# Performance work log

Hardware: AMD Instinct MI355X
Metric: run time of the kernel (lower is better)

The kernel has to match this reference:

```python
import jax, jax.numpy as jnp
import numpy as np

T = 2048          # tokens (single causal prefill sequence)
H = 4096          # hidden_size
NH = 32           # num query heads
NKV = 8           # num kv heads (GQA)
HD = H // NH      # head_dim = 128
ROPE_THETA = 500000.0
Q_SIZE = NH * HD
KV_SIZE = NKV * HD


def setup_inputs() -> dict:
    key = jax.random.key(0)
    k1, k2, k3 = jax.random.split(key, 3)
    return {
        "positions": jnp.arange(T, dtype=jnp.int32),
        "hidden_states": jax.random.normal(k1, (T, H), dtype=jnp.float32) * 0.02,
        "w_qkv": jax.random.normal(k2, (H, Q_SIZE + 2 * KV_SIZE), dtype=jnp.float32) * (1.0 / np.sqrt(H)),
        "w_o": jax.random.normal(k3, (Q_SIZE, H), dtype=jnp.float32) * (1.0 / np.sqrt(Q_SIZE)),
    }


def _apply_rope(x, positions):
    # x: [T, heads, HD]; neox-style (non-interleaved) RoPE as in get_rope
    half = HD // 2
    inv_freq = 1.0 / (ROPE_THETA ** (jnp.arange(0, half, dtype=jnp.float32) / half * 1.0))
    # note: standard llama uses arange(0, HD, 2)/HD == arange(half)/half
    freqs = positions.astype(jnp.float32)[:, None] * inv_freq[None, :]   # [T, half]
    cos = jnp.cos(freqs)[:, None, :]  # [T, 1, half]
    sin = jnp.sin(freqs)[:, None, :]
    x1, x2 = x[..., :half], x[..., half:]
    return jnp.concatenate([x1 * cos - x2 * sin, x2 * cos + x1 * sin], axis=-1).astype(x.dtype)


def reference(positions, hidden_states, w_qkv, w_o):
    # qkv_proj (no bias)
    qkv = hidden_states @ w_qkv                               # [T, 6144]
    q, k, v = jnp.split(qkv, [Q_SIZE, Q_SIZE + KV_SIZE], axis=-1)
    q = q.reshape(T, NH, HD)
    k = k.reshape(T, NKV, HD)
    v = v.reshape(T, NKV, HD)

    # fused RoPE on q and k (k would be written rotated into the KV cache)
    q = _apply_rope(q, positions)
    k = _apply_rope(k, positions)

    # GQA: expand kv heads to query heads
    group = NH // NKV
    k_rep = jnp.repeat(k, group, axis=1)                      # [T, NH, HD]
    v_rep = jnp.repeat(v, group, axis=1)

    scale = HD ** -0.5
    scores = jnp.einsum('qhd,shd->hqs', q, k_rep) * scale     # [NH, T, T]
    causal = jnp.tril(jnp.ones((T, T), dtype=bool))
    scores = jnp.where(causal[None], scores, jnp.finfo(scores.dtype).min)
    probs = jax.nn.softmax(scores, axis=-1)
    attn = jnp.einsum('hqs,shd->qhd', probs, v_rep)           # [T, NH, HD]

    out = attn.reshape(T, Q_SIZE) @ w_o                       # o_proj
    return out
```

## Files before the change

### kernel.cpp

```cpp
#include <hip/hip_runtime.h>
#include <cstdint>
#include <cstddef>

#define T_SEQ 2048
#define H_DIM 4096
#define NH 32
#define NKV 8
#define HD 128
#define QKV_N 6144
#define Q_SIZE 4096
#define KV_SIZE 1024

typedef __attribute__((ext_vector_type(8))) short bf16x8;
typedef __attribute__((ext_vector_type(4))) short short4v;
typedef __attribute__((ext_vector_type(4))) float f32x4;

__device__ __forceinline__ short f2bf(float f) {
  union { float f; uint32_t u; } v; v.f = f;
  uint32_t r = v.u + 0x7fffu + ((v.u >> 16) & 1u);
  return (short)(r >> 16);
}

__device__ __forceinline__ void gload_lds16(const void* g, void* l) {
  __builtin_amdgcn_global_load_lds((const __attribute__((address_space(1))) void*)g,
                                   (__attribute__((address_space(3))) void*)l,
                                   16, 0, 0);
}

__global__ __launch_bounds__(256) void cvt_bf16_kernel(const float* __restrict__ in,
                                                       short* __restrict__ out, int n4) {
  int i = blockIdx.x * 256 + threadIdx.x;
  if (i < n4) {
    float4 v = ((const float4*)in)[i];
    short4v s;
    s.x = f2bf(v.x); s.y = f2bf(v.y); s.z = f2bf(v.z); s.w = f2bf(v.w);
    ((short4v*)out)[i] = s;
  }
}

__global__ __launch_bounds__(256) void transpose_cvt_kernel(const float* __restrict__ in,
                                                            short* __restrict__ out,
                                                            int rows, int cols) {
  __shared__ float tile[32][33];
  int bx = blockIdx.x * 32;
  int by = blockIdx.y * 32;
  int x = threadIdx.x, y = threadIdx.y;
#pragma unroll
  for (int i = 0; i < 32; i += 8)
    tile[y + i][x] = in[(size_t)(by + y + i) * cols + bx + x];
  __syncthreads();
#pragma unroll
  for (int i = 0; i < 32; i += 8)
    out[(size_t)(bx + y + i) * rows + by + x] = f2bf(tile[x][y + i]);
}

__global__ __launch_bounds__(256) void gemm_bt_kernel(const short* __restrict__ A,
                                                      const short* __restrict__ Bt,
                                                      float* __restrict__ C,
                                                      int M, int N, int K) {
  __shared__ short As[128 * 32];
  __shared__ short Bs[128 * 32];
  int tid = threadIdx.x;
  int w = tid >> 6, lane = tid & 63;
  int quad = lane >> 4, l16 = lane & 15;
  int wm = (w >> 1) * 64, wn = (w & 1) * 64;
  int bm = blockIdx.y * 128, bn = blockIdx.x * 128;
  f32x4 acc[4][4] = {};
  for (int kk = 0; kk < K; kk += 32) {
    __syncthreads();
#pragma unroll
    for (int p = 0; p < 2; ++p) {
      int e = (p * 256 + tid) * 8;
      int row = e >> 5, kc = e & 31;
      gload_lds16(A + (size_t)(bm + row) * K + kk + kc, As + e);
      gload_lds16(Bt + (size_t)(bn + row) * K + kk + kc, Bs + e);
    }
    __syncthreads();
    bf16x8 af[4], bfr[4];
#pragma unroll
    for (int mi = 0; mi < 4; ++mi)
      af[mi] = *(const bf16x8*)(As + (wm + mi * 16 + l16) * 32 + quad * 8);
#pragma unroll
    for (int ni = 0; ni < 4; ++ni)
      bfr[ni] = *(const bf16x8*)(Bs + (wn + ni * 16 + l16) * 32 + quad * 8);
#pragma unroll
    for (int mi = 0; mi < 4; ++mi)
#pragma unroll
      for (int ni = 0; ni < 4; ++ni)
        acc[mi][ni] = __builtin_amdgcn_mfma_f32_16x16x32_bf16(af[mi], bfr[ni], acc[mi][ni], 0, 0, 0);
  }
#pragma unroll
  for (int mi = 0; mi < 4; ++mi)
#pragma unroll
    for (int ni = 0; ni < 4; ++ni) {
      int r0 = bm + wm + mi * 16 + quad * 4;
      int c0 = bn + wn + ni * 16 + l16;
#pragma unroll
      for (int r = 0; r < 4; ++r)
        C[(size_t)(r0 + r) * N + c0] = acc[mi][ni][r];
    }
}

__global__ __launch_bounds__(256) void rope_kernel(const float* __restrict__ qkv,
                                                   const int* __restrict__ positions,
                                                   short* __restrict__ qb,
                                                   short* __restrict__ kb) {
  int t = blockIdx.x;
  int hh = blockIdx.y * 4 + (threadIdx.x >> 6);
  int j = threadIdx.x & 63;
  float pos = (float)positions[t];
  float f = pos * exp2f(-(float)j * 0.29580575889569017f);
  float c = cosf(f), sn = sinf(f);
  size_t rowbase = (size_t)t * QKV_N;
  int coloff = (hh < NH) ? hh * HD : Q_SIZE + (hh - NH) * HD;
  float x1 = qkv[rowbase + coloff + j];
  float x2 = qkv[rowbase + coloff + j + 64];
  float o1 = x1 * c - x2 * sn;
  float o2 = x2 * c + x1 * sn;
  const float scale2 = 0.08838834764831845f * 1.4426950408889634f;
  short* dst;
  if (hh < NH) {
    o1 *= scale2; o2 *= scale2;
    dst = qb + ((size_t)hh * T_SEQ + t) * HD;
  } else {
    dst = kb + ((size_t)(hh - NH) * T_SEQ + t) * HD;
  }
  dst[j] = f2bf(o1);
  dst[j + 64] = f2bf(o2);
}

__global__ __launch_bounds__(256) void transpose_v_kernel(const float* __restrict__ qkv,
                                                          short* __restrict__ vt) {
  __shared__ float tile[32][33];
  int bx = blockIdx.x * 32;
  int by = blockIdx.y * 32;
  int x = threadIdx.x, y = threadIdx.y;
#pragma unroll
  for (int i = 0; i < 32; i += 8)
    tile[y + i][x] = qkv[(size_t)(by + y + i) * QKV_N + (Q_SIZE + KV_SIZE) + bx + x];
  __syncthreads();
#pragma unroll
  for (int i = 0; i < 32; i += 8)
    vt[(size_t)(bx + y + i) * T_SEQ + by + x] = f2bf(tile[x][y + i]);
}

#define PS_STR 72
__global__ __launch_bounds__(256, 2) void flash_kernel(const short* __restrict__ qb,
                                                       const short* __restrict__ kb,
                                                       const short* __restrict__ vt,
                                                       short* __restrict__ attn) {
  __shared__ short Ks[64 * 128];
  __shared__ short Vs[128 * 64];
  __shared__ short Ps[8][16 * PS_STR];
  int c = (int)gridDim.x - 1 - (int)blockIdx.x;
  int h = blockIdx.y;
  int kvh = h >> 2;
  int tid = threadIdx.x;
  int w = tid >> 6, lane = tid & 63;
  int quad = lane >> 4, l16 = lane & 15;
  int qrow0w = c * 128 + w * 32;

  const short* kbh = kb + (size_t)kvh * T_SEQ * HD;
  const short* vth = vt + (size_t)kvh * HD * T_SEQ;

  bf16x8 qf[2][4];
#pragma unroll
  for (int g = 0; g < 2; ++g) {
    const short* qbase = qb + ((size_t)h * T_SEQ + qrow0w + g * 16 + l16) * HD + quad * 8;
#pragma unroll
    for (int dk = 0; dk < 4; ++dk) qf[g][dk] = *(const bf16x8*)(qbase + dk * 32);
  }
  f32x4 o[2][8] = {};
  float lp[2] = {0.0f, 0.0f};

  int ktmax_blk = 2 * c + 2;
  int ktmax_w = 2 * c + 1 + (w >> 1);

  for (int kt = 0; kt < ktmax_blk; ++kt) {
    int kpos0 = kt * 64;
    __syncthreads();
#pragma unroll
    for (int p4 = 0; p4 < 4; ++p4) {
      int e = p4 * 256 + tid;
      int kr = e >> 4, kp = e & 15;
      gload_lds16(kbh + (size_t)(kpos0 + kr) * HD + ((kp ^ (kr & 7)) * 8), Ks + e * 8);
      int vd = e >> 3, vp = e & 7;
      gload_lds16(vth + (size_t)vd * T_SEQ + kpos0 + ((vp ^ (vd & 7)) * 8), Vs + e * 8);
    }
    __syncthreads();
    if (kt >= ktmax_w) continue;

    f32x4 s[2][4] = {};
#pragma unroll
    for (int mi = 0; mi < 4; ++mi) {
      int kr = mi * 16 + l16;
      const short* kfb = Ks + kr * 128;
      int sw = kr & 7;
#pragma unroll
      for (int dk = 0; dk < 4; ++dk) {
        bf16x8 kf = *(const bf16x8*)(kfb + (((dk * 4 + quad) ^ sw) * 8));
        s[0][mi] = __builtin_amdgcn_mfma_f32_16x16x32_bf16(kf, qf[0][dk], s[0][mi], 0, 0, 0);
        s[1][mi] = __builtin_amdgcn_mfma_f32_16x16x32_bf16(kf, qf[1][dk], s[1][mi], 0, 0, 0);
      }
    }
#pragma unroll
    for (int g = 0; g < 2; ++g) {
      int qr = qrow0w + g * 16 + l16;
      bool need_mask = (kpos0 + 63 > qrow0w + g * 16);
#pragma unroll
      for (int mi = 0; mi < 4; ++mi) {
        float p0, p1, p2, p3;
        if (need_mask) {
          int kp = kpos0 + mi * 16 + quad * 4;
          p0 = exp2f((kp + 0 > qr) ? -1e30f : s[g][mi][0]);
          p1 = exp2f((kp + 1 > qr) ? -1e30f : s[g][mi][1]);
          p2 = exp2f((kp + 2 > qr) ? -1e30f : s[g][mi][2]);
          p3 = exp2f((kp + 3 > qr) ? -1e30f : s[g][mi][3]);
        } else {
          p0 = exp2f(s[g][mi][0]); p1 = exp2f(s[g][mi][1]);
          p2 = exp2f(s[g][mi][2]); p3 = exp2f(s[g][mi][3]);
        }
        lp[g] += p0 + p1 + p2 + p3;
        short4v pk;
        pk.x = f2bf(p0); pk.y = f2bf(p1); pk.z = f2bf(p2); pk.w = f2bf(p3);
        *(short4v*)(&Ps[w * 2 + g][l16 * PS_STR + mi * 16 + quad * 4]) = pk;
      }
    }
#pragma unroll
    for (int kf2 = 0; kf2 < 2; ++kf2) {
      bf16x8 pf0 = *(const bf16x8*)(&Ps[w * 2 + 0][l16 * PS_STR + kf2 * 32 + quad * 8]);
      bf16x8 pf1 = *(const bf16x8*)(&Ps[w * 2 + 1][l16 * PS_STR + kf2 * 32 + quad * 8]);
#pragma unroll
      for (int ni = 0; ni < 8; ++ni) {
        int vd = ni * 16 + l16;
        bf16x8 vf = *(const bf16x8*)(Vs + vd * 64 + (((kf2 * 4 + quad) ^ (vd & 7)) * 8));
        o[0][ni] = __builtin_amdgcn_mfma_f32_16x16x32_bf16(vf, pf0, o[0][ni], 0, 0, 0);
        o[1][ni] = __builtin_amdgcn_mfma_f32_16x16x32_bf16(vf, pf1, o[1][ni], 0, 0, 0);
      }
    }
  }
#pragma unroll
  for (int g = 0; g < 2; ++g) {
    float lt = lp[g];
    lt += __shfl_xor(lt, 16, 64);
    lt += __shfl_xor(lt, 32, 64);
    float rl = 1.0f / lt;
    short* dst = attn + (size_t)(qrow0w + g * 16 + l16) * Q_SIZE + h * HD + quad * 4;
#pragma unroll
    for (int ni = 0; ni < 8; ++ni) {
      short4v ov;
      ov.x = f2bf(o[g][ni][0] * rl); ov.y = f2bf(o[g][ni][1] * rl);
      ov.z = f2bf(o[g][ni][2] * rl); ov.w = f2bf(o[g][ni][3] * rl);
      *(short4v*)(dst + ni * 16) = ov;
    }
  }
}

extern "C" void kernel_launch(void* const* d_in, const int* in_sizes, int n_in,
                              void* d_out, int out_size, void* d_ws, size_t ws_size,
                              hipStream_t stream) {
  const int* positions = (const int*)d_in[0];
  const float* hidden  = (const float*)d_in[1];
  const float* w_qkv   = (const float*)d_in[2];
  const float* w_o     = (const float*)d_in[3];
  float* out = (float*)d_out;

  char* p = (char*)d_ws;
  short* hA    = (short*)p;               short* attn = hA;
  p += (size_t)T_SEQ * H_DIM * 2;
  short* wqkvT = (short*)p;
  p += (size_t)QKV_N * H_DIM * 2;
  float* qkv   = (float*)p;               short* woT = (short*)p;
  short* qb = wqkvT;
  short* kb = qb + (size_t)NH * T_SEQ * HD;
  short* vt = kb + (size_t)NKV * T_SEQ * HD;

  cvt_bf16_kernel<<<dim3(T_SEQ * H_DIM / 4 / 256), 256, 0, stream>>>(hidden, hA, T_SEQ * H_DIM / 4);
  transpose_cvt_kernel<<<dim3(QKV_N / 32, H_DIM / 32), dim3(32, 8), 0, stream>>>(w_qkv, wqkvT, H_DIM, QKV_N);
  gemm_bt_kernel<<<dim3(QKV_N / 128, T_SEQ / 128), 256, 0, stream>>>(hA, wqkvT, qkv, T_SEQ, QKV_N, H_DIM);
  rope_kernel<<<dim3(T_SEQ, (NH + NKV) / 4), 256, 0, stream>>>(qkv, positions, qb, kb);
  transpose_v_kernel<<<dim3(KV_SIZE / 32, T_SEQ / 32), dim3(32, 8), 0, stream>>>(qkv, vt);
  transpose_cvt_kernel<<<dim3(H_DIM / 32, H_DIM / 32), dim3(32, 8), 0, stream>>>(w_o, woT, H_DIM, H_DIM);
  flash_kernel<<<dim3(T_SEQ / 128, NH), 256, 0, stream>>>(qb, kb, vt, attn);
  gemm_bt_kernel<<<dim3(H_DIM / 128, T_SEQ / 128), 256, 0, stream>>>(attn, woT, out, T_SEQ, H_DIM, H_DIM);
}
```

Baseline: 584.7 us.

## Fuse RoPE, scaling and V transpose into QKV GEMM epilogue

Replaces the generic QKV GEMM plus separate RoPE and V-transpose kernels with a dedicated GEMM whose column tiles map to one head each. The epilogue applies RoPE with fast sincos, folds in the softmax scale for Q, and writes bf16 Q/K/V (V transposed) directly. Each warp's column assignment is arranged so that the pairs (d, d+64) sit in the same thread's registers. This removes the fp32 QKV intermediate round trip and two kernel launches, but it relies on __sincosf precision for large positions and on strided epilogue stores.

```diff
diff --git a/kernel.cpp b/kernel.cpp
--- a/kernel.cpp
+++ b/kernel.cpp
@@ -101,47 +101,92 @@
     }
 }
 
-__global__ __launch_bounds__(256) void rope_kernel(const float* __restrict__ qkv,
-                                                   const int* __restrict__ positions,
-                                                   short* __restrict__ qb,
-                                                   short* __restrict__ kb) {
-  int t = blockIdx.x;
-  int hh = blockIdx.y * 4 + (threadIdx.x >> 6);
-  int j = threadIdx.x & 63;
-  float pos = (float)positions[t];
-  float f = pos * exp2f(-(float)j * 0.29580575889569017f);
-  float c = cosf(f), sn = sinf(f);
-  size_t rowbase = (size_t)t * QKV_N;
-  int coloff = (hh < NH) ? hh * HD : Q_SIZE + (hh - NH) * HD;
-  float x1 = qkv[rowbase + coloff + j];
-  float x2 = qkv[rowbase + coloff + j + 64];
-  float o1 = x1 * c - x2 * sn;
-  float o2 = x2 * c + x1 * sn;
+__global__ __launch_bounds__(256) void qkv_gemm_kernel(const short* __restrict__ A,
+                                                       const short* __restrict__ Bt,
+                                                       const int* __restrict__ positions,
+                                                       short* __restrict__ qb,
+                                                       short* __restrict__ kb,
+                                                       short* __restrict__ vt) {
+  __shared__ short As[128 * 32];
+  __shared__ short Bs[128 * 32];
+  const int K = H_DIM;
+  int tid = threadIdx.x;
+  int w = tid >> 6, lane = tid & 63;
+  int quad = lane >> 4, l16 = lane & 15;
+  int wm = (w >> 1) * 64;
+  int cgb = (w & 1) * 32;
+  int cb = blockIdx.x;
+  int bm = blockIdx.y * 128, bn = cb * 128;
+  f32x4 acc[4][4] = {};
+  for (int kk = 0; kk < K; kk += 32) {
+    __syncthreads();
+#pragma unroll
+    for (int p = 0; p < 2; ++p) {
+      int e = (p * 256 + tid) * 8;
+      int row = e >> 5, kc = e & 31;
+      gload_lds16(A + (size_t)(bm + row) * K + kk + kc, As + e);
+      gload_lds16(Bt + (size_t)(bn + row) * K + kk + kc, Bs + e);
+    }
+    __syncthreads();
+    bf16x8 af[4], bfr[4];
+#pragma unroll
+    for (int mi = 0; mi < 4; ++mi)
+      af[mi] = *(const bf16x8*)(As + (wm + mi * 16 + l16) * 32 + quad * 8);
+#pragma unroll
+    for (int nj = 0; nj < 4; ++nj) {
+      int cg = cgb + (nj & 1) * 16 + (nj >> 1) * 64;
+      bfr[nj] = *(const bf16x8*)(Bs + (cg + l16) * 32 + quad * 8);
+    }
+#pragma unroll
+    for (int mi = 0; mi < 4; ++mi)
+#pragma unroll
+      for (int nj = 0; nj < 4; ++nj)
+        acc[mi][nj] = __builtin_amdgcn_mfma_f32_16x16x32_bf16(af[mi], bfr[nj], acc[mi][nj], 0, 0, 0);
+  }
   const float scale2 = 0.08838834764831845f * 1.4426950408889634f;
-  short* dst;
-  if (hh < NH) {
-    o1 *= scale2; o2 *= scale2;
-    dst = qb + ((size_t)hh * T_SEQ + t) * HD;
+  if (cb < NH + NKV) {
+    short* dstbase;
+    float qs;
+    if (cb < NH) { dstbase = qb + (size_t)cb * T_SEQ * HD; qs = scale2; }
+    else         { dstbase = kb + (size_t)(cb - NH) * T_SEQ * HD; qs = 1.0f; }
+    float invf[2];
+#pragma unroll
+    for (int nj = 0; nj < 2; ++nj)
+      invf[nj] = exp2f(-(float)(cgb + nj * 16 + l16) * 0.29580575889569017f);
+#pragma unroll
+    for (int mi = 0; mi < 4; ++mi) {
+#pragma unroll
+      for (int r = 0; r < 4; ++r) {
+        int t = bm + wm + mi * 16 + quad * 4 + r;
+        float pos = (float)positions[t];
+#pragma unroll
+        for (int nj = 0; nj < 2; ++nj) {
+          float f = pos * invf[nj];
+          float sn, cs;
+          __sincosf(f, &sn, &cs);
+          float x1 = acc[mi][nj][r], x2 = acc[mi][nj + 2][r];
+          float o1 = (x1 * cs - x2 * sn) * qs;
+          float o2 = (x2 * cs + x1 * sn) * qs;
+          int d = cgb + nj * 16 + l16;
+          dstbase[(size_t)t * HD + d] = f2bf(o1);
+          dstbase[(size_t)t * HD + d + 64] = f2bf(o2);
+        }
+      }
+    }
   } else {
-    dst = kb + ((size_t)(hh - NH) * T_SEQ + t) * HD;
-  }
-  dst[j] = f2bf(o1);
-  dst[j + 64] = f2bf(o2);
-}
-
-__global__ __launch_bounds__(256) void transpose_v_kernel(const float* __restrict__ qkv,
-                                                          short* __restrict__ vt) {
-  __shared__ float tile[32][33];
-  int bx = blockIdx.x * 32;
-  int by = blockIdx.y * 32;
-  int x = threadIdx.x, y = threadIdx.y;
-#pragma unroll
-  for (int i = 0; i < 32; i += 8)
-    tile[y + i][x] = qkv[(size_t)(by + y + i) * QKV_N + (Q_SIZE + KV_SIZE) + bx + x];
-  __syncthreads();
-#pragma unroll
-  for (int i = 0; i < 32; i += 8)
-    vt[(size_t)(bx + y + i) * T_SEQ + by + x] = f2bf(tile[x][y + i]);
+    short* vb = vt + (size_t)(cb - NH - NKV) * HD * T_SEQ;
+#pragma unroll
+    for (int mi = 0; mi < 4; ++mi)
+#pragma unroll
+      for (int nj = 0; nj < 4; ++nj) {
+        int d = cgb + (nj & 1) * 16 + (nj >> 1) * 64 + l16;
+        int t0 = bm + wm + mi * 16 + quad * 4;
+        short4v pk;
+        pk.x = f2bf(acc[mi][nj][0]); pk.y = f2bf(acc[mi][nj][1]);
+        pk.z = f2bf(acc[mi][nj][2]); pk.w = f2bf(acc[mi][nj][3]);
+        *(short4v*)(vb + (size_t)d * T_SEQ + t0) = pk;
+      }
+  }
 }
 
 #define PS_STR 72
@@ -268,18 +313,15 @@
   char* p = (char*)d_ws;
   short* hA    = (short*)p;               short* attn = hA;
   p += (size_t)T_SEQ * H_DIM * 2;
-  short* wqkvT = (short*)p;
+  short* wqkvT = (short*)p;               short* woT = wqkvT;
   p += (size_t)QKV_N * H_DIM * 2;
-  float* qkv   = (float*)p;               short* woT = (short*)p;
-  short* qb = wqkvT;
+  short* qb = (short*)p;
   short* kb = qb + (size_t)NH * T_SEQ * HD;
   short* vt = kb + (size_t)NKV * T_SEQ * HD;
 
   cvt_bf16_kernel<<<dim3(T_SEQ * H_DIM / 4 / 256), 256, 0, stream>>>(hidden, hA, T_SEQ * H_DIM / 4);
   transpose_cvt_kernel<<<dim3(QKV_N / 32, H_DIM / 32), dim3(32, 8), 0, stream>>>(w_qkv, wqkvT, H_DIM, QKV_N);
-  gemm_bt_kernel<<<dim3(QKV_N / 128, T_SEQ / 128), 256, 0, stream>>>(hA, wqkvT, qkv, T_SEQ, QKV_N, H_DIM);
-  rope_kernel<<<dim3(T_SEQ, (NH + NKV) / 4), 256, 0, stream>>>(qkv, positions, qb, kb);
-  transpose_v_kernel<<<dim3(KV_SIZE / 32, T_SEQ / 32), dim3(32, 8), 0, stream>>>(qkv, vt);
+  qkv_gemm_kernel<<<dim3(QKV_N / 128, T_SEQ / 128), 256, 0, stream>>>(hA, wqkvT, positions, qb, kb, vt);
   transpose_cvt_kernel<<<dim3(H_DIM / 32, H_DIM / 32), dim3(32, 8), 0, stream>>>(w_o, woT, H_DIM, H_DIM);
   flash_kernel<<<dim3(T_SEQ / 128, NH), 256, 0, stream>>>(qb, kb, vt, attn);
   gemm_bt_kernel<<<dim3(H_DIM / 128, T_SEQ / 128), 256, 0, stream>>>(attn, woT, out, T_SEQ, H_DIM, H_DIM);
```

New measurement: 593.6 us. About the same (+1.5%).
